# Kernel tuning notes

Measured on AMD Instinct MI355X. Metric: run time of the kernel, lower is better.

## Reference

```python
import jax, jax.numpy as jnp
import numpy as np

B, F, S, P, E, H = 64, 32, 512, 96, 8, 2048
TOP_K = 2
ALPHA = 10.0
ENT_EPS = 1e-8
CV_EPS = 1e-10


def setup_inputs() -> dict:
    key = jax.random.key(0)
    ks = jax.random.split(key, 8)
    s = 0.02
    return {
        "x": jax.random.normal(ks[0], (B, F, S), dtype=jnp.float32),
        "time_embedding": jax.random.normal(ks[1], (B, F, S), dtype=jnp.float32),
        "Wg": jax.random.normal(ks[2], (S, E), dtype=jnp.float32) * s,
        "bg": jnp.zeros((E,), dtype=jnp.float32),
        "W1": jax.random.normal(ks[3], (E, S, H), dtype=jnp.float32) * s,
        "b1": jnp.zeros((E, H), dtype=jnp.float32),
        "W2": jax.random.normal(ks[4], (E, H, P), dtype=jnp.float32) * s,
        "b2": jnp.zeros((E, P), dtype=jnp.float32),
    }


def _gates(tf, Wg, bg):
    # tf: [F, B, S] -> logits [F, B, E]
    logits = jnp.einsum('fbs,se->fbe', tf, Wg) + bg
    # kthvalue(x, E - top_k + 1) = (E - top_k)-th entry (0-based) of ascending sort = k-th largest
    kth = jnp.sort(logits, axis=-1)[..., E - TOP_K]  # [F, B]
    mask = logits < kth[..., None]
    sm = jax.nn.softmax(logits, axis=-1)
    dec = jnp.where(mask, ALPHA * jnp.log(sm + 1.0), ALPHA * (jnp.exp(sm) - 1.0))
    return jax.nn.softmax(dec, axis=-1)  # [F, B, E]


def reference(x, time_embedding, Wg, bg, W1, b1, W2, b2):
    xf = jnp.transpose(x, (1, 0, 2))               # [F, B, S]
    tf = jnp.transpose(time_embedding, (1, 0, 2))  # [F, B, S]
    gates = _gates(tf, Wg, bg)                     # [F, B, E]

    # all experts on all features (eval mode: dropout = identity)
    h = jax.nn.gelu(jnp.einsum('fbs,esh->febh', xf, W1) + b1[None, :, None, :], approximate=False)
    eo = jnp.einsum('febh,ehp->febp', h, W2) + b2[None, :, None, :]  # [F, E, B, P]
    out = jnp.einsum('fbe,febp->fbp', gates, eo)   # gated weighted sum
    output = jnp.transpose(out, (1, 0, 2))         # [B, F, P]

    # selector loss: cv_squared of importance = gates.sum(batch) expanded over pred_len
    gsum = gates.sum(axis=1)                       # [F, E]
    imp = jnp.broadcast_to(gsum[..., None], (F, E, P)).reshape(F, E * P)
    cv = jnp.var(imp, axis=1, ddof=1) / (jnp.mean(imp, axis=1) ** 2 + CV_EPS)
    selector_loss = jnp.sum(cv)                    # loss_coef = 1.0

    # entropy loss: importance1 = gates.mean(batch) expanded over pred_len
    gmean = gates.mean(axis=1)                     # [F, E]
    imp1 = jnp.broadcast_to(gmean[..., None], (F, E, P))
    entropy_loss = jnp.sum((-imp1 * jnp.log(imp1 + ENT_EPS)).mean(axis=(1, 2)))

    return output, selector_loss, entropy_loss
```

## Files before the change

kernel.cpp:

```cpp
#include <hip/hip_runtime.h>
#include <math.h>

#define B_ 64
#define F_ 32
#define S_ 512
#define P_ 96
#define E_ 8
#define H_ 2048
#define M_ 2048

#define BM 256
#define BH 128
#define BK 64
#define ZSPLIT 4
#define HPZ (H_ / ZSPLIT)
#define NHT (HPZ / BH)
#define NKC (S_ / BK)

typedef __bf16 bf16x8 __attribute__((ext_vector_type(8)));
typedef __bf16 bf16x4 __attribute__((ext_vector_type(4)));
typedef float f32x4 __attribute__((ext_vector_type(4)));

#define MFMA16(a, b, c) __builtin_amdgcn_mfma_f32_16x16x32_bf16((a), (b), (c), 0, 0, 0)

#define GLL16(gp, lp) __builtin_amdgcn_global_load_lds(                     \
    (const __attribute__((address_space(1))) void*)(gp),                    \
    (__attribute__((address_space(3))) void*)(lp), 16, 0, 0)

__device__ __forceinline__ float fast_gelu(float x) {
  float e = __builtin_amdgcn_exp2f(-2.45546696f * x);
  return x * __builtin_amdgcn_rcpf(1.0f + e);
}

#define PREP_GRID 3776

__global__ __launch_bounds__(256) void k_prep(const float* __restrict__ x,
                                              const float* __restrict__ te,
                                              const float* __restrict__ Wg,
                                              const float* __restrict__ bg,
                                              const float* __restrict__ W1,
                                              const float* __restrict__ W2,
                                              __bf16* __restrict__ xbf,
                                              __bf16* __restrict__ w1t,
                                              __bf16* __restrict__ w2t,
                                              float* __restrict__ gates,
                                              float* __restrict__ out) {
  __shared__ float tile[64 * 65];
  const int blk = blockIdx.x;
  const int tid = threadIdx.x;

  if (blk < 2048) {
    int e = blk >> 8, tt = blk & 255;
    int si = tt >> 5, hi = tt & 31;
    const float* src = W1 + (size_t)e * S_ * H_ + (size_t)(si * 64) * H_ + hi * 64;
    {
      int row = tid >> 2;
      int cb = (tid & 3) * 16;
#pragma unroll
      for (int k = 0; k < 4; ++k) {
        f32x4 v = *(const f32x4*)(src + (size_t)row * H_ + cb + k * 4);
#pragma unroll
        for (int u = 0; u < 4; ++u) tile[row * 65 + cb + k * 4 + u] = v[u];
      }
    }
    __syncthreads();
    {
      int h = tid >> 2;
      int sb = (tid & 3) * 16;
      __bf16* dst = w1t + (size_t)e * H_ * S_ + (size_t)(hi * 64 + h) * S_ + si * 64 + sb;
      bf16x8 o0, o1;
#pragma unroll
      for (int k = 0; k < 8; ++k) o0[k] = (__bf16)tile[(sb + k) * 65 + h];
#pragma unroll
      for (int k = 0; k < 8; ++k) o1[k] = (__bf16)tile[(sb + 8 + k) * 65 + h];
      *(bf16x8*)dst = o0;
      *(bf16x8*)(dst + 8) = o1;
    }
    return;
  }
  if (blk < 2560) {
    int t = blk - 2048;
    int e = t >> 6, hi = (t >> 1) & 31, ph = t & 1;
    const float* src = W2 + (size_t)e * H_ * P_ + (size_t)(hi * 64) * P_ + ph * 48;
    {
      int h = tid & 63;
      int seg = tid >> 6;
#pragma unroll
      for (int k = 0; k < 3; ++k) {
        f32x4 v = *(const f32x4*)(src + (size_t)h * P_ + seg * 12 + k * 4);
#pragma unroll
        for (int u = 0; u < 4; ++u) tile[h * 49 + seg * 12 + k * 4 + u] = v[u];
      }
    }
    __syncthreads();
    if (tid < 192) {
      int p = tid >> 2;
      int hb = (tid & 3) * 16;
      __bf16* dst = w2t + (size_t)e * P_ * H_ + (size_t)(ph * 48 + p) * H_ + hi * 64 + hb;
      bf16x8 o0, o1;
#pragma unroll
      for (int k = 0; k < 8; ++k) o0[k] = (__bf16)tile[(hb + k) * 49 + p];
#pragma unroll
      for (int k = 0; k < 8; ++k) o1[k] = (__bf16)tile[(hb + 8 + k) * 49 + p];
      *(bf16x8*)dst = o0;
      *(bf16x8*)(dst + 8) = o1;
    }
    return;
  }
  if (blk < 3072) {
    size_t i = (size_t)(blk - 2560) * 2048 + (size_t)tid * 8;
#pragma unroll
    for (int k = 0; k < 2; ++k) {
      f32x4 v = *(const f32x4*)(x + i + k * 4);
      bf16x4 o = {(__bf16)v[0], (__bf16)v[1], (__bf16)v[2], (__bf16)v[3]};
      *(bf16x4*)(xbf + i + k * 4) = o;
    }
    return;
  }
  if (blk < 3584) {
    int wave = tid >> 6, lane = tid & 63;
    int m = (blk - 3072) * 4 + wave;
    const float* trow = te + (size_t)m * S_;
    float acc[E_];
#pragma unroll
    for (int e = 0; e < E_; ++e) acc[e] = 0.f;
    for (int s = lane; s < S_; s += 64) {
      float t = trow[s];
      const f32x4* wgr = (const f32x4*)(Wg + s * E_);
      f32x4 a = wgr[0], b = wgr[1];
      acc[0] += t * a[0]; acc[1] += t * a[1]; acc[2] += t * a[2]; acc[3] += t * a[3];
      acc[4] += t * b[0]; acc[5] += t * b[1]; acc[6] += t * b[2]; acc[7] += t * b[3];
    }
#pragma unroll
    for (int e = 0; e < E_; ++e) {
#pragma unroll
      for (int off = 32; off > 0; off >>= 1) acc[e] += __shfl_xor(acc[e], off, 64);
    }
    if (lane == 0) {
      float lg[E_];
      float m1 = -3.4e38f, m2 = -3.4e38f;
#pragma unroll
      for (int e = 0; e < E_; ++e) {
        float v = acc[e] + bg[e];
        lg[e] = v;
        if (v > m1) { m2 = m1; m1 = v; }
        else if (v > m2) { m2 = v; }
      }
      float den = 0.f, sm[E_];
#pragma unroll
      for (int e = 0; e < E_; ++e) { sm[e] = expf(lg[e] - m1); den += sm[e]; }
      float inv = 1.f / den;
      float dmax = -3.4e38f, dec[E_];
#pragma unroll
      for (int e = 0; e < E_; ++e) {
        float p = sm[e] * inv;
        float d = (lg[e] < m2) ? (10.f * logf(p + 1.f)) : (10.f * (expf(p) - 1.f));
        dec[e] = d;
        dmax = fmaxf(dmax, d);
      }
      float dden = 0.f;
#pragma unroll
      for (int e = 0; e < E_; ++e) { dec[e] = expf(dec[e] - dmax); dden += dec[e]; }
      float dinv = 1.f / dden;
#pragma unroll
      for (int e = 0; e < E_; ++e) gates[m * E_ + e] = dec[e] * dinv;
    }
    return;
  }
  {
    size_t i = (size_t)(blk - 3584) * 1024 + (size_t)tid * 4;
    f32x4 z4 = {0.f, 0.f, 0.f, 0.f};
    *(f32x4*)(out + i) = z4;
  }
}

__global__ __launch_bounds__(512, 1) void k_experts(
    const __bf16* __restrict__ xbf,
    const __bf16* __restrict__ w1t,
    const __bf16* __restrict__ w2t,
    const float* __restrict__ b1,
    const float* __restrict__ b2,
    const float* __restrict__ gates,
    float* __restrict__ out)
{
  __shared__ __align__(16) __bf16 W1s[2][BH * BK];
  __shared__ __align__(16) __bf16 Xs[2][BM * BK];
  __shared__ __align__(16) __bf16 Hs[BM * BH];

  const int tid = threadIdx.x;

  if (blockIdx.z == ZSPLIT) {
    if (blockIdx.x != 0 || blockIdx.y != 0) return;
    float* gsum = (float*)&Hs[0];
    float* cvs  = gsum + F_ * E_;
    float* ents = cvs + F_;
    if (tid < 256) {
      int f = tid >> 3, ee = tid & 7;
      float s = 0.f;
      for (int b = 0; b < B_; ++b) s += gates[(size_t)(b * F_ + f) * E_ + ee];
      gsum[f * E_ + ee] = s;
    }
    __syncthreads();
    if (tid < F_) {
      float mean = 0.f;
#pragma unroll
      for (int k = 0; k < E_; ++k) mean += gsum[tid * E_ + k];
      mean *= (1.f / E_);
      float ss = 0.f;
#pragma unroll
      for (int k = 0; k < E_; ++k) { float d = gsum[tid * E_ + k] - mean; ss += d * d; }
      float var = (float)P_ * ss / (float)(E_ * P_ - 1);
      cvs[tid] = var / (mean * mean + 1e-10f);
      float ent = 0.f;
#pragma unroll
      for (int k = 0; k < E_; ++k) { float g = gsum[tid * E_ + k] * (1.f / B_); ent += -g * logf(g + 1e-8f); }
      ents[tid] = ent * (1.f / E_);
    }
    __syncthreads();
    if (tid == 0) {
      float a = 0.f, b = 0.f;
      for (int k = 0; k < F_; ++k) { a += cvs[k]; b += ents[k]; }
      out[(size_t)M_ * P_ + 0] = a;
      out[(size_t)M_ * P_ + 1] = b;
    }
    return;
  }

  const int wave = tid >> 6, lane = tid & 63;
  const int l15 = lane & 15, quad = lane >> 4;
  const int e = blockIdx.x;
  const int m0 = blockIdx.y * BM;
  const int hz = blockIdx.z * HPZ;

  const int sg = lane & 7;
  const int srl = lane >> 3;
  const int gcol = ((sg ^ srl) * 8);

  const __bf16* w1base = w1t + ((size_t)e * H_ + hz + wave * 16 + srl) * S_ + gcol;
  const __bf16* xg = xbf + (size_t)(m0 + wave * 32 + srl) * S_ + gcol;
  const __bf16* w2z = w2t + (size_t)e * P_ * H_ + hz;

  const int hq = (wave & 1) * 64;
  const int mq = (wave >> 1) * 64;
  const int w32 = wave * 32;

  const f32x4 fz = {0.f, 0.f, 0.f, 0.f};
  f32x4 acc1[4][4];
  f32x4 acc2[2][6];
#pragma unroll
  for (int rt = 0; rt < 2; ++rt)
#pragma unroll
    for (int j = 0; j < 6; ++j) acc2[rt][j] = fz;

  auto STAGE = [&](int ht_, int kc_, int b) {
    const __bf16* w1p = w1base + (size_t)(ht_ * BH) * S_ + kc_ * BK;
    const __bf16* xp  = xg + kc_ * BK;
#pragma unroll
    for (int p = 0; p < 2; ++p)
      GLL16(w1p + (size_t)(p * 8) * S_, &W1s[b][(wave * 16 + p * 8) * BK]);
#pragma unroll
    for (int p = 0; p < 4; ++p)
      GLL16(xp + (size_t)(p * 8) * S_, &Xs[b][(wave * 32 + p * 8) * BK]);
  };

  auto COMPUTE = [&](int b) {
#pragma unroll
    for (int kk = 0; kk < 2; ++kk) {
      bf16x8 af[4], bx[4];
#pragma unroll
      for (int i = 0; i < 4; ++i) {
        int r = hq + i * 16 + l15;
        af[i] = *(const bf16x8*)&W1s[b][r * BK + (((kk * 4 + quad) ^ (r & 7)) * 8)];
      }
#pragma unroll
      for (int j = 0; j < 4; ++j) {
        int r = mq + j * 16 + l15;
        bx[j] = *(const bf16x8*)&Xs[b][r * BK + (((kk * 4 + quad) ^ (r & 7)) * 8)];
      }
#pragma unroll
      for (int i = 0; i < 4; ++i)
#pragma unroll
        for (int j = 0; j < 4; ++j)
          acc1[i][j] = MFMA16(af[i], bx[j], acc1[i][j]);
    }
  };

  auto GEMM2Q = [&](int htc, int kk) {
    bf16x8 a0, a1;
    {
      int ab0 = (w32 + l15) * 256 + (((kk * 4 + quad) ^ l15) * 16);
      int ab1 = (w32 + 16 + l15) * 256 + (((kk * 4 + quad) ^ l15) * 16);
      a0 = *(const bf16x8*)((const char*)Hs + ab0);
      a1 = *(const bf16x8*)((const char*)Hs + ab1);
    }
#pragma unroll
    for (int j = 0; j < 6; ++j) {
      bf16x8 bb = *(const bf16x8*)(w2z + (size_t)(j * 16 + l15) * H_ + htc * BH + kk * 32 + quad * 8);
      acc2[0][j] = MFMA16(a0, bb, acc2[0][j]);
      acc2[1][j] = MFMA16(a1, bb, acc2[1][j]);
    }
  };

  auto GELU = [&](int ht_) {
    const float* b1w = b1 + (size_t)e * H_ + hz + ht_ * BH;
#pragma unroll
    for (int i = 0; i < 4; ++i) {
      int h = hq + i * 16 + quad * 4;
      f32x4 bv = *(const f32x4*)(b1w + h);
#pragma unroll
      for (int j = 0; j < 4; ++j) {
        bf16x4 hv;
#pragma unroll
        for (int r = 0; r < 4; ++r)
          hv[r] = (__bf16)fast_gelu(acc1[i][j][r] + bv[r]);
        int m = mq + j * 16 + l15;
        int wb = m * 256 + (((h >> 3) ^ l15) * 16) + (quad & 1) * 8;
        *(bf16x4*)((char*)Hs + wb) = hv;
      }
    }
  };

  STAGE(0, 0, 0);
  __syncthreads();

  for (int ht = 0; ht < NHT; ++ht) {
#pragma unroll
    for (int i = 0; i < 4; ++i)
#pragma unroll
      for (int j = 0; j < 4; ++j) acc1[i][j] = fz;

    int bsel = 0;
#pragma unroll
    for (int kc = 0; kc < NKC; ++kc) {
      if (kc < NKC - 1) {
        STAGE(ht, kc + 1, bsel ^ 1);
      } else if (ht < NHT - 1) {
        STAGE(ht + 1, 0, bsel ^ 1);
      }
      if (kc < 4 && ht > 0) GEMM2Q(ht - 1, kc);

      COMPUTE(bsel);
      __syncthreads();
      bsel ^= 1;
    }
    GELU(ht);
    __syncthreads();
  }
#pragma unroll
  for (int kk = 0; kk < 4; ++kk) GEMM2Q(NHT - 1, kk);

#pragma unroll
  for (int rt = 0; rt < 2; ++rt) {
#pragma unroll
    for (int r = 0; r < 4; ++r) {
      int m = m0 + w32 + rt * 16 + quad * 4 + r;
      float g = gates[m * E_ + e];
#pragma unroll
      for (int j = 0; j < 6; ++j) {
        int col = j * 16 + l15;
        float v = acc2[rt][j][r];
        if (blockIdx.z == 0) v += b2[e * P_ + col];
        atomicAdd(&out[(size_t)m * P_ + col], g * v);
      }
    }
  }
}

extern "C" void kernel_launch(void* const* d_in, const int* in_sizes, int n_in,
                              void* d_out, int out_size, void* d_ws, size_t ws_size,
                              hipStream_t stream) {
  const float* x  = (const float*)d_in[0];
  const float* te = (const float*)d_in[1];
  const float* Wg = (const float*)d_in[2];
  const float* bg = (const float*)d_in[3];
  const float* W1 = (const float*)d_in[4];
  const float* b1 = (const float*)d_in[5];
  const float* W2 = (const float*)d_in[6];
  const float* b2 = (const float*)d_in[7];
  float* out = (float*)d_out;

  char* ws = (char*)d_ws;
  float* gates = (float*)ws;
  __bf16* xbf  = (__bf16*)(ws + 65536);
  __bf16* w1t  = (__bf16*)(ws + 65536 + 2097152);
  __bf16* w2t  = (__bf16*)(ws + 65536 + 2097152 + 16777216);

  k_prep<<<PREP_GRID, 256, 0, stream>>>(x, te, Wg, bg, W1, W2, xbf, w1t, w2t, gates, out);
  k_experts<<<dim3(E_, M_ / BM, ZSPLIT + 1), 512, 0, stream>>>(xbf, w1t, w2t, b1, b2, gates, out);
}
```

Measured before the change: 217.1 us.

## Double expert-kernel block to 1024 threads with smaller per-wave tiles

The expert GEMM block grows from 8 to 16 waves, and each wave's work shrinks. Each wave now owns a 32x64 GEMM1 sub-tile and one 16-row slice for GEMM2, so per-thread accumulators and staging loads are halved. The aim is more latency hiding and MFMA issue parallelism per CU while keeping the same tile sizes and shared memory. The trade-off is more waves contending at each barrier and lower register reuse per MFMA operand. The Hs swizzle is adjusted to use the row's low bits, and the epilogue is rewritten for the new mapping.

```diff
diff --git a/kernel.cpp b/kernel.cpp
--- a/kernel.cpp
+++ b/kernel.cpp
@@ -174,7 +174,7 @@
   }
 }
 
-__global__ __launch_bounds__(512, 1) void k_experts(
+__global__ __launch_bounds__(1024) void k_experts(
     const __bf16* __restrict__ xbf,
     const __bf16* __restrict__ w1t,
     const __bf16* __restrict__ w2t,
@@ -236,39 +236,35 @@
   const int srl = lane >> 3;
   const int gcol = ((sg ^ srl) * 8);
 
-  const __bf16* w1base = w1t + ((size_t)e * H_ + hz + wave * 16 + srl) * S_ + gcol;
-  const __bf16* xg = xbf + (size_t)(m0 + wave * 32 + srl) * S_ + gcol;
+  const __bf16* w1base = w1t + ((size_t)e * H_ + hz + wave * 8 + srl) * S_ + gcol;
+  const __bf16* xg = xbf + (size_t)(m0 + wave * 16 + srl) * S_ + gcol;
   const __bf16* w2z = w2t + (size_t)e * P_ * H_ + hz;
 
-  const int hq = (wave & 1) * 64;
-  const int mq = (wave >> 1) * 64;
-  const int w32 = wave * 32;
+  const int hq = (wave & 3) * 32;
+  const int mq = (wave >> 2) * 64;
+  const int mt = wave;
 
   const f32x4 fz = {0.f, 0.f, 0.f, 0.f};
-  f32x4 acc1[4][4];
-  f32x4 acc2[2][6];
-#pragma unroll
-  for (int rt = 0; rt < 2; ++rt)
-#pragma unroll
-    for (int j = 0; j < 6; ++j) acc2[rt][j] = fz;
+  f32x4 acc1[2][4];
+  f32x4 acc2[6];
+#pragma unroll
+  for (int j = 0; j < 6; ++j) acc2[j] = fz;
 
   auto STAGE = [&](int ht_, int kc_, int b) {
     const __bf16* w1p = w1base + (size_t)(ht_ * BH) * S_ + kc_ * BK;
     const __bf16* xp  = xg + kc_ * BK;
+    GLL16(w1p, &W1s[b][(wave * 8) * BK]);
 #pragma unroll
     for (int p = 0; p < 2; ++p)
-      GLL16(w1p + (size_t)(p * 8) * S_, &W1s[b][(wave * 16 + p * 8) * BK]);
-#pragma unroll
-    for (int p = 0; p < 4; ++p)
-      GLL16(xp + (size_t)(p * 8) * S_, &Xs[b][(wave * 32 + p * 8) * BK]);
+      GLL16(xp + (size_t)(p * 8) * S_, &Xs[b][(wave * 16 + p * 8) * BK]);
   };
 
   auto COMPUTE = [&](int b) {
 #pragma unroll
     for (int kk = 0; kk < 2; ++kk) {
-      bf16x8 af[4], bx[4];
-#pragma unroll
-      for (int i = 0; i < 4; ++i) {
+      bf16x8 af[2], bx[4];
+#pragma unroll
+      for (int i = 0; i < 2; ++i) {
         int r = hq + i * 16 + l15;
         af[i] = *(const bf16x8*)&W1s[b][r * BK + (((kk * 4 + quad) ^ (r & 7)) * 8)];
       }
@@ -278,7 +274,7 @@
         bx[j] = *(const bf16x8*)&Xs[b][r * BK + (((kk * 4 + quad) ^ (r & 7)) * 8)];
       }
 #pragma unroll
-      for (int i = 0; i < 4; ++i)
+      for (int i = 0; i < 2; ++i)
 #pragma unroll
         for (int j = 0; j < 4; ++j)
           acc1[i][j] = MFMA16(af[i], bx[j], acc1[i][j]);
@@ -286,25 +282,19 @@
   };
 
   auto GEMM2Q = [&](int htc, int kk) {
-    bf16x8 a0, a1;
-    {
-      int ab0 = (w32 + l15) * 256 + (((kk * 4 + quad) ^ l15) * 16);
-      int ab1 = (w32 + 16 + l15) * 256 + (((kk * 4 + quad) ^ l15) * 16);
-      a0 = *(const bf16x8*)((const char*)Hs + ab0);
-      a1 = *(const bf16x8*)((const char*)Hs + ab1);
-    }
+    int ab = (mt * 16 + l15) * 256 + (((kk * 4 + quad) ^ l15) * 16);
+    bf16x8 a = *(const bf16x8*)((const char*)Hs + ab);
 #pragma unroll
     for (int j = 0; j < 6; ++j) {
       bf16x8 bb = *(const bf16x8*)(w2z + (size_t)(j * 16 + l15) * H_ + htc * BH + kk * 32 + quad * 8);
-      acc2[0][j] = MFMA16(a0, bb, acc2[0][j]);
-      acc2[1][j] = MFMA16(a1, bb, acc2[1][j]);
+      acc2[j] = MFMA16(a, bb, acc2[j]);
     }
   };
 
   auto GELU = [&](int ht_) {
     const float* b1w = b1 + (size_t)e * H_ + hz + ht_ * BH;
 #pragma unroll
-    for (int i = 0; i < 4; ++i) {
+    for (int i = 0; i < 2; ++i) {
       int h = hq + i * 16 + quad * 4;
       f32x4 bv = *(const f32x4*)(b1w + h);
 #pragma unroll
@@ -314,7 +304,7 @@
         for (int r = 0; r < 4; ++r)
           hv[r] = (__bf16)fast_gelu(acc1[i][j][r] + bv[r]);
         int m = mq + j * 16 + l15;
-        int wb = m * 256 + (((h >> 3) ^ l15) * 16) + (quad & 1) * 8;
+        int wb = m * 256 + (((h >> 3) ^ (m & 15)) * 16) + (quad & 1) * 8;
         *(bf16x4*)((char*)Hs + wb) = hv;
       }
     }
@@ -325,7 +315,7 @@
 
   for (int ht = 0; ht < NHT; ++ht) {
 #pragma unroll
-    for (int i = 0; i < 4; ++i)
+    for (int i = 0; i < 2; ++i)
 #pragma unroll
       for (int j = 0; j < 4; ++j) acc1[i][j] = fz;
 
@@ -350,18 +340,15 @@
   for (int kk = 0; kk < 4; ++kk) GEMM2Q(NHT - 1, kk);
 
 #pragma unroll
-  for (int rt = 0; rt < 2; ++rt) {
-#pragma unroll
-    for (int r = 0; r < 4; ++r) {
-      int m = m0 + w32 + rt * 16 + quad * 4 + r;
-      float g = gates[m * E_ + e];
-#pragma unroll
-      for (int j = 0; j < 6; ++j) {
-        int col = j * 16 + l15;
-        float v = acc2[rt][j][r];
-        if (blockIdx.z == 0) v += b2[e * P_ + col];
-        atomicAdd(&out[(size_t)m * P_ + col], g * v);
-      }
+  for (int r = 0; r < 4; ++r) {
+    int m = m0 + mt * 16 + quad * 4 + r;
+    float g = gates[m * E_ + e];
+#pragma unroll
+    for (int j = 0; j < 6; ++j) {
+      int col = j * 16 + l15;
+      float v = acc2[j][r];
+      if (blockIdx.z == 0) v += b2[e * P_ + col];
+      atomicAdd(&out[(size_t)m * P_ + col], g * v);
     }
   }
 }
@@ -386,5 +373,5 @@
   __bf16* w2t  = (__bf16*)(ws + 65536 + 2097152 + 16777216);
 
   k_prep<<<PREP_GRID, 256, 0, stream>>>(x, te, Wg, bg, W1, W2, xbf, w1t, w2t, gates, out);
-  k_experts<<<dim3(E_, M_ / BM, ZSPLIT + 1), 512, 0, stream>>>(xbf, w1t, w2t, b1, b2, gates, out);
+  k_experts<<<dim3(E_, M_ / BM, ZSPLIT + 1), 1024, 0, stream>>>(xbf, w1t, w2t, b1, b2, gates, out);
 }
```

Measured after the change: 224.8 us. +3.6%, slower.
